# Kernel optimization log

Measured on AMD Instinct MI355X. Metric: run time of the kernel, lower is better.

The kernel has to match this reference:

```python
import jax, jax.numpy as jnp
import numpy as np

B, S, N = 16, 128, 64            # batch, sentence length, padded KB-word slots per sentence
E, DK, H, L = 128, 128, 128, 32  # char embed, kb embed, per-direction hidden (hidden_size=2H), labels
CHAR_NUM, KB_NUM = 8000, 200000


def setup_inputs():
    key = jax.random.key(0)
    ks = jax.random.split(key, 40)
    u = lambda k, sh: jax.random.uniform(k, sh, jnp.float32, -0.08, 0.08)
    inp = {
        "char_ids": jax.random.randint(ks[0], (B, S), 0, CHAR_NUM),
        "kb_word_ids": jax.random.randint(ks[1], (B, N), 0, KB_NUM),
        "word_begin": jax.random.randint(ks[2], (B, N), 0, S),
        "word_len": jax.random.randint(ks[3], (B, N), 0, 6),
        "label": jax.random.randint(ks[4], (B, S), 0, L),
        "sequence_length": jax.random.randint(ks[5], (B,), S // 2, S + 1),
        "char_emb": u(ks[6], (CHAR_NUM, E)),
        "kb_emb": u(ks[7], (KB_NUM, DK)),
        "dense_W": u(ks[8], (2 * H, L)),
        "dense_b": jnp.zeros((L,), jnp.float32),
        "crf_T": u(ks[9], (L, L)),
    }
    i = 10
    for p in ("f", "r"):
        inp[p + "_Wcx"] = u(ks[i], (E, 4 * H))
        inp[p + "_Wch"] = u(ks[i + 1], (H, 4 * H))
        inp[p + "_bc"] = jnp.zeros((4 * H,), jnp.float32)
        inp[p + "_Wwx"] = u(ks[i + 2], (DK, 3 * H))
        inp[p + "_Wwh"] = u(ks[i + 3], (H, 3 * H))
        inp[p + "_bw"] = jnp.zeros((3 * H,), jnp.float32)
        inp[p + "_Wlx"] = u(ks[i + 4], (E, H))
        inp[p + "_Wlc"] = u(ks[i + 5], (H, H))
        inp[p + "_bl"] = jnp.zeros((H,), jnp.float32)
        i += 6
    return inp


def _lattice_dir(X, Xw, begin, end, pos_valid, word_valid,
                 Wcx, Wch, bc, Wwx, Wwh, bw, Wlx, Wlc, bl):
    # X:[S,E] chars in scan order, Xw:[N,DK] KB words, begin/end:[N] span indices
    # in scan order (end inclusive), pos_valid:[S] bool, word_valid:[N] bool.
    Xg = X @ Wcx + bc    # [S,4H] hoisted char-gate input projection
    Xl = X @ Wlx + bl    # [S,H]  hoisted link-gate input projection
    Wg = Xw @ Wwx + bw   # [N,3H] hoisted word-gate input projection

    def step(carry, t):
        h_hist, c_hist = carry                 # [S+1,H]; slot k = state after step k-1
        h_prev, c_prev = h_hist[t], c_hist[t]
        gi, gf, go, gg = jnp.split(Xg[t] + h_prev @ Wch, 4)
        i = jax.nn.sigmoid(gi); f = jax.nn.sigmoid(gf)
        o = jax.nn.sigmoid(go); g = jnp.tanh(gg)
        # word cells: built from the state just before each word's begin position
        hb, cb = h_hist[begin], c_hist[begin]  # [N,H]
        wi, wf, wg = jnp.split(Wg + hb @ Wwh, 3, axis=1)
        cw = jax.nn.sigmoid(wf) * cb + jax.nn.sigmoid(wi) * jnp.tanh(wg)  # [N,H]
        lg = jax.nn.sigmoid(Xl[t] + cw @ Wlc)  # [N,H] link gates
        wmask = ((end == t) & word_valid).astype(X.dtype)[:, None]
        ew = jnp.exp(lg) * wmask
        ec = jnp.exp(i)
        c_lat = (ec * g + (ew * cw).sum(0)) / (ec + ew.sum(0))  # gate-normalized merge
        c_std = f * c_prev + i * g             # plain LSTM step when no word ends at t
        c_t = jnp.where(wmask.sum() > 0, c_lat, c_std)
        h_t = o * jnp.tanh(c_t)
        v = pos_valid[t]
        h_hist = h_hist.at[t + 1].set(jnp.where(v, h_t, h_prev))
        c_hist = c_hist.at[t + 1].set(jnp.where(v, c_t, c_prev))
        return (h_hist, c_hist), jnp.where(v, h_t, jnp.zeros_like(h_t))

    init = (jnp.zeros((S + 1, H), X.dtype), jnp.zeros((S + 1, H), X.dtype))
    _, hs = jax.lax.scan(step, init, jnp.arange(S))
    return hs  # [S,H]


def _forward(char_ids, kb_word_ids, word_begin, word_len, label, sequence_length,
             char_emb, kb_emb, dense_W, dense_b, crf_T, fparams, rparams):
    X = char_emb[char_ids]            # [B,S,E]
    Xw = kb_emb[kb_word_ids]          # [B,N,DK]
    end = jnp.minimum(word_begin + word_len, S - 1)   # inclusive span end
    word_valid = end < sequence_length[:, None]       # whole span inside sentence
    pos = jnp.arange(S)
    pv_f = pos[None, :] < sequence_length[:, None]
    fwd = jax.vmap(lambda x, xw, b, e, pv, wv:
                   _lattice_dir(x, xw, b, e, pv, wv, *fparams))(
        X, Xw, word_begin, end, pv_f, word_valid)
    # backward direction: flip time axis; span (b,e) maps to (S-1-e, S-1-b)
    pv_r = pos[None, :] >= (S - sequence_length)[:, None]
    bwd = jax.vmap(lambda x, xw, b, e, pv, wv:
                   _lattice_dir(x, xw, b, e, pv, wv, *rparams))(
        X[:, ::-1], Xw, S - 1 - end, S - 1 - word_begin, pv_r, word_valid)[:, ::-1]
    feats = jnp.concatenate([fwd, bwd], axis=-1)      # [B,S,2H]
    logits = feats @ dense_W + dense_b                # [B,S,L]
    # CRF negative log-likelihood
    mask = pv_f.astype(logits.dtype)                  # [B,S]
    emit = jnp.take_along_axis(logits, label[..., None], axis=2)[..., 0]
    trans = crf_T[label[:, :-1], label[:, 1:]]
    gold = (emit * mask).sum(1) + (trans * mask[:, 1:]).sum(1)

    def fstep(alpha, xs):
        logit_t, m_t = xs
        new = jax.scipy.special.logsumexp(alpha[:, :, None] + crf_T[None], axis=1) + logit_t
        return jnp.where(m_t[:, None] > 0, new, alpha), None

    alpha, _ = jax.lax.scan(fstep, logits[:, 0],
                            (logits[:, 1:].transpose(1, 0, 2), mask[:, 1:].T))
    logZ = jax.scipy.special.logsumexp(alpha, axis=1)
    return jnp.mean(logZ - gold)


def reference(char_ids, kb_word_ids, word_begin, word_len, label, sequence_length,
              char_emb, kb_emb, dense_W, dense_b, crf_T,
              f_Wcx, f_Wch, f_bc, f_Wwx, f_Wwh, f_bw, f_Wlx, f_Wlc, f_bl,
              r_Wcx, r_Wch, r_bc, r_Wwx, r_Wwh, r_bw, r_Wlx, r_Wlc, r_bl):
    fparams = (f_Wcx, f_Wch, f_bc, f_Wwx, f_Wwh, f_bw, f_Wlx, f_Wlc, f_bl)
    rparams = (r_Wcx, r_Wch, r_bc, r_Wwx, r_Wwh, r_bw, r_Wlx, r_Wlc, r_bl)
    return _forward(char_ids, kb_word_ids, word_begin, word_len, label, sequence_length,
                    char_emb, kb_emb, dense_W, dense_b, crf_T, fparams, rparams)
```

## Files before the change

kernel.cpp:

```cpp
#include <hip/hip_runtime.h>


typedef _Float16 f16x8 __attribute__((ext_vector_type(8)));
typedef float    f32x4 __attribute__((ext_vector_type(4)));

__device__ __forceinline__ float sigm(float x) { return 1.f / (1.f + __expf(-x)); }
__device__ __forceinline__ float tanh_fast(float x) {
    return 1.f - 2.f / (__expf(2.f * x) + 1.f);
}
__device__ __forceinline__ void bar_lgkm() {
    asm volatile("s_waitcnt lgkmcnt(0)\n\ts_barrier" ::: "memory");
}

__device__ __forceinline__ f32x4 mfma16(f16x8 a, f16x8 b, f32x4 c) {
    return __builtin_amdgcn_mfma_f32_16x16x32_f16(a, b, c, 0, 0, 0);
}

template <int K, int J, int RPB, int BLK>
__global__ __launch_bounds__(BLK)
void gemm_pair(const float* __restrict__ emb, const int* __restrict__ idx,
               const float* __restrict__ W0, const float* __restrict__ W1,
               const float* __restrict__ b0, const float* __restrict__ b1,
               float* __restrict__ out, int rowsTotal, int Sdim, int revmode)
{
    constexpr int NJ4 = J / 4;
    constexpr int RT  = BLK / NJ4;
    constexpr int RPT = RPB / RT;
    static_assert(BLK % NJ4 == 0 && RPB % RT == 0, "layout");
    const int y = blockIdx.y;
    const float* __restrict__ W    = y ? W1 : W0;
    const float* __restrict__ bias = y ? b1 : b0;
    float* __restrict__ outp = out + (size_t)y * rowsTotal * J;
    const int rev = (revmode && y) ? 1 : 0;

    __shared__ __align__(16) float xs[RPB * K];
    __shared__ const float* srcs[RPB];
    const int tid = threadIdx.x;
    const int r0 = blockIdx.x * RPB;
    if (tid < RPB) {
        const int row = r0 + tid;
        const float* s = nullptr;
        if (row < rowsTotal) {
            if (idx) {
                const int bb = row / Sdim, tt = row - bb * Sdim;
                const int ts = rev ? (Sdim - 1 - tt) : tt;
                s = emb + (size_t)idx[bb * Sdim + ts] * K;
            } else {
                s = emb + (size_t)row * K;
            }
        }
        srcs[tid] = s;
    }
    __syncthreads();
    constexpr int NQ = RPB * K / 4;
    for (int q = tid; q < NQ; q += BLK) {
        const int rr = q / (K / 4), qq = q - rr * (K / 4);
        const float4* s = (const float4*)srcs[rr];
        ((float4*)xs)[q] = s ? s[qq] : make_float4(0.f, 0.f, 0.f, 0.f);
    }
    __syncthreads();

    const int jq = tid % NJ4;
    const int rg = tid / NJ4;
    float4 acc[RPT];
#pragma unroll
    for (int r = 0; r < RPT; ++r) acc[r] = make_float4(0.f, 0.f, 0.f, 0.f);
    const float4* __restrict__ W4 = (const float4*)W;
#pragma unroll 4
    for (int k = 0; k < K; ++k) {
        const float4 wv = W4[(size_t)k * NJ4 + jq];
#pragma unroll
        for (int r = 0; r < RPT; ++r) {
            const float xv = xs[(rg * RPT + r) * K + k];
            acc[r].x = fmaf(xv, wv.x, acc[r].x);
            acc[r].y = fmaf(xv, wv.y, acc[r].y);
            acc[r].z = fmaf(xv, wv.z, acc[r].z);
            acc[r].w = fmaf(xv, wv.w, acc[r].w);
        }
    }
    const float4 bv = ((const float4*)bias)[jq];
#pragma unroll
    for (int r = 0; r < RPT; ++r) {
        const int row = r0 + rg * RPT + r;
        if (row < rowsTotal)
            ((float4*)outp)[(size_t)row * NJ4 + jq] =
                make_float4(acc[r].x + bv.x, acc[r].y + bv.y,
                            acc[r].z + bv.z, acc[r].w + bv.w);
    }
}

#define HH_BYTES (129 * 128 * 2)
#define CH_BYTES (129 * 128 * 4)
#define LAT_DYN_SMEM (HH_BYTES + CH_BYTES)

__global__ __launch_bounds__(512, 2)
void lattice_kernel(const float* __restrict__ Xg,
                    const float* __restrict__ Xl,
                    const float* __restrict__ Wgp,
                    const float* __restrict__ Wch_f, const float* __restrict__ Wch_r,
                    const float* __restrict__ Wwh_f, const float* __restrict__ Wwh_r,
                    const float* __restrict__ Wlc_f, const float* __restrict__ Wlc_r,
                    const int* __restrict__ word_begin, const int* __restrict__ word_len,
                    const int* __restrict__ seqlen,
                    float* __restrict__ feats)
{
    extern __shared__ __align__(16) char dyn_smem[];
    _Float16* hh = (_Float16*)dyn_smem;
    float*    ch = (float*)(dyn_smem + HH_BYTES);

    const int bdid = blockIdx.x;
    const int b = bdid >> 1, dir = bdid & 1;
    const int tid = threadIdx.x;
    const int wid = tid >> 6;
    const int ln  = tid & 63;
    const int lg  = ln >> 4;
    const int jm  = wid * 16 + (ln & 15);

    const float* Wch = dir ? Wch_r : Wch_f;
    const float* Wwh = dir ? Wwh_r : Wwh_f;
    const float* Wlc = dir ? Wlc_r : Wlc_f;

    f16x8 Bc[4][4];
#pragma unroll
    for (int g = 0; g < 4; ++g)
#pragma unroll
        for (int kt = 0; kt < 4; ++kt) {
            f16x8 v;
#pragma unroll
            for (int i = 0; i < 8; ++i)
                v[i] = (_Float16)Wch[(size_t)(kt * 32 + lg * 8 + i) * 512 + (g * 128 + jm)];
            Bc[g][kt] = v;
        }
    f16x8 Bw[3][4];
#pragma unroll
    for (int p = 0; p < 3; ++p)
#pragma unroll
        for (int kt = 0; kt < 4; ++kt) {
            f16x8 v;
#pragma unroll
            for (int i = 0; i < 8; ++i)
                v[i] = (_Float16)Wwh[(size_t)(kt * 32 + lg * 8 + i) * 384 + (p * 128 + jm)];
            Bw[p][kt] = v;
        }
    f16x8 Bl[4];
#pragma unroll
    for (int kt = 0; kt < 4; ++kt) {
        f16x8 v;
#pragma unroll
        for (int i = 0; i < 8; ++i)
            v[i] = (_Float16)Wlc[(size_t)(kt * 32 + lg * 8 + i) * 128 + jm];
        Bl[kt] = v;
    }

    __shared__ __align__(16) _Float16 cw2s[2][2][128];
    __shared__ int ev_start[129];
    __shared__ int cnts[128];
    __shared__ int fills[128];
    __shared__ short ev_word[64];
    __shared__ short wbeg_s[64];

    const int sl = seqlen[b];

    if (tid < 128) { cnts[tid] = 0; fills[tid] = 0; }
    __syncthreads();
    int myvalid = 0, myed = 0;
    if (tid < 64) {
        const int bg = word_begin[b * 64 + tid];
        const int lnw = word_len[b * 64 + tid];
        int ef = bg + lnw; if (ef > 127) ef = 127;
        myvalid = (ef < sl);
        const int bd_ = dir ? (127 - ef) : bg;
        const int ed_ = dir ? (127 - bg) : ef;
        wbeg_s[tid] = (short)bd_;
        myed = ed_;
        if (myvalid) atomicAdd(&cnts[ed_], 1);
    }
    __syncthreads();
    if (tid == 0) {
        int run = 0; ev_start[0] = 0;
        for (int t = 0; t < 128; ++t) { run += cnts[t]; ev_start[t + 1] = run; }
    }
    __syncthreads();
    if (tid < 64 && myvalid) {
        const int pos = atomicAdd(&fills[myed], 1);
        ev_word[ev_start[myed] + pos] = (short)tid;
    }
    if (tid < 128) { hh[tid] = (_Float16)0.f; ch[tid] = 0.f; }
    __syncthreads();

    const float* Xg_b = Xg + ((size_t)dir * 2048 + (size_t)b * 128) * 512;
    const float* Xl_b = Xl + ((size_t)dir * 2048 + (size_t)b * 128) * 128;
    const float* Wg_b = Wgp + ((size_t)dir * 1024 + (size_t)b * 64) * 384;

    float h_reg = 0.f, c_reg = 0.f;

    int   curE, cur_ec0;
    int   cur_bgs[2] = {0, 0};
    float cur_wgp[2][3] = {};
    float cur_xl = 0.f;
    float xg_cur[4];
    {
        curE = ev_start[1];
        cur_ec0 = curE < 2 ? curE : 2;
#pragma unroll
        for (int s = 0; s < 2; ++s)
            if (s < cur_ec0) {
                const int wd = ev_word[s];
                cur_bgs[s] = wbeg_s[wd];
                const float* wgr = Wg_b + (size_t)wd * 384;
                cur_wgp[s][0] = wgr[jm];
                cur_wgp[s][1] = wgr[128 + jm];
                cur_wgp[s][2] = wgr[256 + jm];
            }
        if (curE > 0) cur_xl = Xl_b[jm];
#pragma unroll
        for (int g = 0; g < 4; ++g) xg_cur[g] = Xg_b[g * 128 + jm];
    }

    for (int t = 0; t < 128; ++t) {
        int   nxtE = 0, nxt_ec0 = 0;
        int   nxt_bgs[2] = {0, 0};
        float nxt_wgp[2][3] = {};
        float nxt_xl = 0.f;
        float xg_nxt[4] = {0.f, 0.f, 0.f, 0.f};
        if (t < 127) {
            const int e0n = ev_start[t + 1];
            nxtE = ev_start[t + 2] - e0n;
            nxt_ec0 = nxtE < 2 ? nxtE : 2;
#pragma unroll
            for (int s = 0; s < 2; ++s)
                if (s < nxt_ec0) {
                    const int wd = ev_word[e0n + s];
                    nxt_bgs[s] = wbeg_s[wd];
                    const float* wgr = Wg_b + (size_t)wd * 384;
                    nxt_wgp[s][0] = wgr[jm];
                    nxt_wgp[s][1] = wgr[128 + jm];
                    nxt_wgp[s][2] = wgr[256 + jm];
                }
            if (nxtE > 0) nxt_xl = Xl_b[(size_t)(t + 1) * 128 + jm];
#pragma unroll
            for (int g = 0; g < 4; ++g)
                xg_nxt[g] = Xg_b[(size_t)(t + 1) * 512 + g * 128 + jm];
        }

        f16x8 A[4];
#pragma unroll
        for (int kt = 0; kt < 4; ++kt)
            A[kt] = ((const f16x8*)hh)[t * 16 + kt * 4 + lg];
        f32x4 d[4];
#pragma unroll
        for (int g = 0; g < 4; ++g) d[g] = (f32x4){0.f, 0.f, 0.f, 0.f};
#pragma unroll
        for (int kt = 0; kt < 4; ++kt)
#pragma unroll
            for (int g = 0; g < 4; ++g)
                d[g] = mfma16(A[kt], Bc[g][kt], d[g]);

        const float gi = sigm(d[0][0] + xg_cur[0]);
        const float gf = sigm(d[1][0] + xg_cur[1]);
        const float go = sigm(d[2][0] + xg_cur[2]);
        const float gg = tanh_fast(d[3][0] + xg_cur[3]);

        float accn = 0.f, accd = 0.f;
        if (curE > 0) {
            const int e0 = ev_start[t];
            float cwreg[2] = {0.f, 0.f};
#pragma unroll
            for (int s = 0; s < 2; ++s)
                if (s < cur_ec0) {
                    f16x8 Ab[4];
#pragma unroll
                    for (int kt = 0; kt < 4; ++kt)
                        Ab[kt] = ((const f16x8*)hh)[cur_bgs[s] * 16 + kt * 4 + lg];
                    f32x4 ep[3];
#pragma unroll
                    for (int p = 0; p < 3; ++p) ep[p] = (f32x4){0.f, 0.f, 0.f, 0.f};
#pragma unroll
                    for (int kt = 0; kt < 4; ++kt)
#pragma unroll
                        for (int p = 0; p < 3; ++p)
                            ep[p] = mfma16(Ab[kt], Bw[p][kt], ep[p]);
                    const float wi = cur_wgp[s][0] + ep[0][0];
                    const float wf = cur_wgp[s][1] + ep[1][0];
                    const float wv = cur_wgp[s][2] + ep[2][0];
                    const float cb = ch[(size_t)cur_bgs[s] * 128 + jm];
                    const float cwv = sigm(wf) * cb + sigm(wi) * tanh_fast(wv);
                    cwreg[s] = cwv;
                    if (ln < 16) cw2s[0][s][jm] = (_Float16)cwv;
                }
            bar_lgkm();
            const int nc = (curE + 1) >> 1;
            for (int c = 0; c < nc; ++c) {
                const int base2 = c * 2;
                const int en = (curE - base2) < 2 ? (curE - base2) : 2;
                float lgs[2] = {0.f, 0.f};
#pragma unroll
                for (int s = 0; s < 2; ++s)
                    if (s < en) {
                        f16x8 Ac[4];
#pragma unroll
                        for (int kt = 0; kt < 4; ++kt)
                            Ac[kt] = ((const f16x8*)(&cw2s[c & 1][s][0]))[kt * 4 + lg];
                        f32x4 r = (f32x4){0.f, 0.f, 0.f, 0.f};
#pragma unroll
                        for (int kt = 0; kt < 4; ++kt)
                            r = mfma16(Ac[kt], Bl[kt], r);
                        lgs[s] = r[0];
                    }
                const int nb = base2 + 2;
                int nn = curE - nb; nn = nn < 0 ? 0 : (nn > 2 ? 2 : nn);
                float cwn[2] = {0.f, 0.f};
#pragma unroll
                for (int s = 0; s < 2; ++s)
                    if (s < nn) {
                        const int wd = ev_word[e0 + nb + s];
                        const int bg2 = wbeg_s[wd];
                        const float* wgr = Wg_b + (size_t)wd * 384;
                        const float wg0 = wgr[jm], wg1 = wgr[128 + jm], wg2 = wgr[256 + jm];
                        f16x8 Ab[4];
#pragma unroll
                        for (int kt = 0; kt < 4; ++kt)
                            Ab[kt] = ((const f16x8*)hh)[bg2 * 16 + kt * 4 + lg];
                        f32x4 ep[3];
#pragma unroll
                        for (int p = 0; p < 3; ++p) ep[p] = (f32x4){0.f, 0.f, 0.f, 0.f};
#pragma unroll
                        for (int kt = 0; kt < 4; ++kt)
#pragma unroll
                            for (int p = 0; p < 3; ++p)
                                ep[p] = mfma16(Ab[kt], Bw[p][kt], ep[p]);
                        const float wi = wg0 + ep[0][0];
                        const float wf = wg1 + ep[1][0];
                        const float wv = wg2 + ep[2][0];
                        const float cb = ch[(size_t)bg2 * 128 + jm];
                        const float cwv = sigm(wf) * cb + sigm(wi) * tanh_fast(wv);
                        cwn[s] = cwv;
                        if (ln < 16) cw2s[(c + 1) & 1][s][jm] = (_Float16)cwv;
                    }
#pragma unroll
                for (int s = 0; s < 2; ++s)
                    if (s < en) {
                        const float lgv = sigm(cur_xl + lgs[s]);
                        const float ew = __expf(lgv);
                        accn = fmaf(ew, cwreg[s], accn);
                        accd += ew;
                    }
                if (c + 1 < nc) {
                    bar_lgkm();
                    cwreg[0] = cwn[0]; cwreg[1] = cwn[1];
                }
            }
        }

        float c_t;
        if (curE > 0) {
            const float ec = __expf(gi);
            c_t = (ec * gg + accn) / (ec + accd);
        } else {
            c_t = gf * c_reg + gi * gg;
        }
        const float h_t = go * tanh_fast(c_t);
        const bool v = dir ? (t >= 128 - sl) : (t < sl);
        const float hn = v ? h_t : h_reg;
        const float cn = v ? c_t : c_reg;
        h_reg = hn; c_reg = cn;
        if (ln < 16) {
            hh[(size_t)(t + 1) * 128 + jm] = (_Float16)hn;
            ch[(size_t)(t + 1) * 128 + jm] = cn;
        }

        curE = nxtE; cur_ec0 = nxt_ec0;
        cur_bgs[0] = nxt_bgs[0]; cur_bgs[1] = nxt_bgs[1];
#pragma unroll
        for (int s = 0; s < 2; ++s) {
            cur_wgp[s][0] = nxt_wgp[s][0];
            cur_wgp[s][1] = nxt_wgp[s][1];
            cur_wgp[s][2] = nxt_wgp[s][2];
        }
        cur_xl = nxt_xl;
#pragma unroll
        for (int g = 0; g < 4; ++g) xg_cur[g] = xg_nxt[g];
        bar_lgkm();
    }

    for (int i = tid; i < 128 * 128; i += 512) {
        const int t = i >> 7, j = i & 127;
        const bool v = dir ? (t >= 128 - sl) : (t < sl);
        const float hv = v ? (float)hh[(size_t)(t + 1) * 128 + j] : 0.f;
        const int s = dir ? (127 - t) : t;
        feats[((size_t)b * 128 + s) * 256 + dir * 128 + j] = hv;
    }
}

__global__ void crf_kernel(const float* __restrict__ logits,
                           const int* __restrict__ label,
                           const int* __restrict__ seqlen,
                           const float* __restrict__ T,
                           float* __restrict__ out_part)
{
    const int half = threadIdx.x >> 5;
    const int j    = threadIdx.x & 31;
    const int b    = blockIdx.x * 2 + half;

    float Tc[32];
#pragma unroll
    for (int i = 0; i < 32; ++i) Tc[i] = T[i * 32 + j];

    const float* lg = logits + (size_t)b * 128 * 32;
    const int* lab = label + b * 128;
    const int sl = seqlen[b];

    float g = 0.f;
#pragma unroll
    for (int r = 0; r < 4; ++r) {
        const int t = j + r * 32;
        if (t < sl) {
            g += lg[t * 32 + lab[t]];
            if (t >= 1) g += T[lab[t - 1] * 32 + lab[t]];
        }
    }
#pragma unroll
    for (int m = 16; m; m >>= 1) g += __shfl_xor(g, m, 32);

    __shared__ __align__(16) float alpha_s[2][32];
    float av = lg[j];
    alpha_s[half][j] = av;
    __syncthreads();
    for (int t = 1; t < 128; ++t) {
        float a[32];
        const float4* ap = (const float4*)alpha_s[half];
#pragma unroll
        for (int q = 0; q < 8; ++q) {
            const float4 v = ap[q];
            a[4 * q] = v.x; a[4 * q + 1] = v.y; a[4 * q + 2] = v.z; a[4 * q + 3] = v.w;
        }
        float m = -1e30f;
#pragma unroll
        for (int i = 0; i < 32; ++i) m = fmaxf(m, a[i] + Tc[i]);
        float s = 0.f;
#pragma unroll
        for (int i = 0; i < 32; ++i) s += __expf(a[i] + Tc[i] - m);
        float nv = m + __logf(s) + lg[t * 32 + j];
        if (t >= sl) nv = av;
        av = nv;
        __syncthreads();
        alpha_s[half][j] = av;
        __syncthreads();
    }
    float m2 = av;
#pragma unroll
    for (int m = 16; m; m >>= 1) m2 = fmaxf(m2, __shfl_xor(m2, m, 32));
    float s2 = __expf(av - m2);
#pragma unroll
    for (int m = 16; m; m >>= 1) s2 += __shfl_xor(s2, m, 32);
    if (j == 0) out_part[b] = (m2 + __logf(s2)) - g;
}

__global__ void finalize_kernel(const float* __restrict__ partb, float* __restrict__ out)
{
    if (threadIdx.x == 0 && blockIdx.x == 0) {
        float s = 0.f;
        for (int i = 0; i < 16; i++) s += partb[i];
        out[0] = s * (1.f / 16.f);
    }
}

extern "C" void kernel_launch(void* const* d_in, const int* in_sizes, int n_in,
                              void* d_out, int out_size, void* d_ws, size_t ws_size,
                              hipStream_t stream)
{
    (void)in_sizes; (void)n_in; (void)out_size; (void)ws_size;
    const int*   char_ids    = (const int*)d_in[0];
    const int*   kb_word_ids = (const int*)d_in[1];
    const int*   word_begin  = (const int*)d_in[2];
    const int*   word_len    = (const int*)d_in[3];
    const int*   label       = (const int*)d_in[4];
    const int*   seqlen      = (const int*)d_in[5];
    const float* char_emb    = (const float*)d_in[6];
    const float* kb_emb      = (const float*)d_in[7];
    const float* dense_W     = (const float*)d_in[8];
    const float* dense_b     = (const float*)d_in[9];
    const float* crf_T       = (const float*)d_in[10];
    const float* f_Wcx = (const float*)d_in[11];
    const float* f_Wch = (const float*)d_in[12];
    const float* f_bc  = (const float*)d_in[13];
    const float* f_Wwx = (const float*)d_in[14];
    const float* f_Wwh = (const float*)d_in[15];
    const float* f_bw  = (const float*)d_in[16];
    const float* f_Wlx = (const float*)d_in[17];
    const float* f_Wlc = (const float*)d_in[18];
    const float* f_bl  = (const float*)d_in[19];
    const float* r_Wcx = (const float*)d_in[20];
    const float* r_Wch = (const float*)d_in[21];
    const float* r_bc  = (const float*)d_in[22];
    const float* r_Wwx = (const float*)d_in[23];
    const float* r_Wwh = (const float*)d_in[24];
    const float* r_bw  = (const float*)d_in[25];
    const float* r_Wlx = (const float*)d_in[26];
    const float* r_Wlc = (const float*)d_in[27];
    const float* r_bl  = (const float*)d_in[28];

    float* ws = (float*)d_ws;
    size_t o = 0;
    float* Xg     = ws + o; o += (size_t)2 * 2048 * 512;
    float* Xl     = ws + o; o += (size_t)2 * 2048 * 128;
    float* Wg     = ws + o; o += (size_t)2 * 1024 * 384;
    float* feats  = ws + o; o += (size_t)2048 * 256;
    float* logits = ws + o; o += (size_t)2048 * 32;
    float* partb  = ws + o; o += 16;

    gemm_pair<128, 512, 8, 256><<<dim3(256, 2), 256, 0, stream>>>(
        char_emb, char_ids, f_Wcx, r_Wcx, f_bc, r_bc, Xg, 2048, 128, 1);
    gemm_pair<128, 128, 8, 256><<<dim3(256, 2), 256, 0, stream>>>(
        char_emb, char_ids, f_Wlx, r_Wlx, f_bl, r_bl, Xl, 2048, 128, 1);
    gemm_pair<128, 384, 8, 192><<<dim3(128, 2), 192, 0, stream>>>(
        kb_emb, kb_word_ids, f_Wwx, r_Wwx, f_bw, r_bw, Wg, 1024, 64, 0);

    lattice_kernel<<<32, 512, LAT_DYN_SMEM, stream>>>(
        Xg, Xl, Wg, f_Wch, r_Wch, f_Wwh, r_Wwh, f_Wlc, r_Wlc,
        word_begin, word_len, seqlen, feats);

    gemm_pair<256, 32, 16, 128><<<dim3(128, 1), 128, 0, stream>>>(
        feats, nullptr, dense_W, dense_W, dense_b, dense_b, logits, 2048, 128, 0);
    crf_kernel<<<8, 64, 0, stream>>>(logits, label, seqlen, crf_T, partb);
    finalize_kernel<<<1, 64, 0, stream>>>(partb, (float*)d_out);
}
```

Before: 518.6 us.

## Halve lattice block to 4 waves, each wave computing two 16-column tiles

The lattice recurrence kernel now runs 256 threads (4 waves) per block instead of 512, and each wave handles two 16-column output tiles. Weight fragments, gate inputs and states are duplicated per tile. Fewer waves should make each per-step barrier cheaper and let every wave reuse its A-operand loads across two MFMAs. The cost is twice the register-held weights per thread, which risks spills, and more serial MFMA and elementwise work per wave on the critical path.

```diff
diff --git a/kernel.cpp b/kernel.cpp
--- a/kernel.cpp
+++ b/kernel.cpp
@@ -93,7 +93,7 @@
 #define CH_BYTES (129 * 128 * 4)
 #define LAT_DYN_SMEM (HH_BYTES + CH_BYTES)
 
-__global__ __launch_bounds__(512, 2)
+__global__ __launch_bounds__(256, 1)
 void lattice_kernel(const float* __restrict__ Xg,
                     const float* __restrict__ Xl,
                     const float* __restrict__ Wgp,
@@ -114,43 +114,54 @@
     const int wid = tid >> 6;
     const int ln  = tid & 63;
     const int lg  = ln >> 4;
-    const int jm  = wid * 16 + (ln & 15);
+    const int c15 = ln & 15;
+    const int jm0 = wid * 32 + c15;
+    const int jm1 = jm0 + 16;
 
     const float* Wch = dir ? Wch_r : Wch_f;
     const float* Wwh = dir ? Wwh_r : Wwh_f;
     const float* Wlc = dir ? Wlc_r : Wlc_f;
 
-    f16x8 Bc[4][4];
+    f16x8 Bc[4][2][4];
 #pragma unroll
     for (int g = 0; g < 4; ++g)
 #pragma unroll
+        for (int ct = 0; ct < 2; ++ct)
+#pragma unroll
+            for (int kt = 0; kt < 4; ++kt) {
+                const int col = g * 128 + (ct ? jm1 : jm0);
+                f16x8 v;
+#pragma unroll
+                for (int i = 0; i < 8; ++i)
+                    v[i] = (_Float16)Wch[(size_t)(kt * 32 + lg * 8 + i) * 512 + col];
+                Bc[g][ct][kt] = v;
+            }
+    f16x8 Bw[3][2][4];
+#pragma unroll
+    for (int p = 0; p < 3; ++p)
+#pragma unroll
+        for (int ct = 0; ct < 2; ++ct)
+#pragma unroll
+            for (int kt = 0; kt < 4; ++kt) {
+                const int col = p * 128 + (ct ? jm1 : jm0);
+                f16x8 v;
+#pragma unroll
+                for (int i = 0; i < 8; ++i)
+                    v[i] = (_Float16)Wwh[(size_t)(kt * 32 + lg * 8 + i) * 384 + col];
+                Bw[p][ct][kt] = v;
+            }
+    f16x8 Bl[2][4];
+#pragma unroll
+    for (int ct = 0; ct < 2; ++ct)
+#pragma unroll
         for (int kt = 0; kt < 4; ++kt) {
+            const int col = ct ? jm1 : jm0;
             f16x8 v;
 #pragma unroll
             for (int i = 0; i < 8; ++i)
-                v[i] = (_Float16)Wch[(size_t)(kt * 32 + lg * 8 + i) * 512 + (g * 128 + jm)];
-            Bc[g][kt] = v;
-        }
-    f16x8 Bw[3][4];
-#pragma unroll
-    for (int p = 0; p < 3; ++p)
-#pragma unroll
-        for (int kt = 0; kt < 4; ++kt) {
-            f16x8 v;
-#pragma unroll
-            for (int i = 0; i < 8; ++i)
-                v[i] = (_Float16)Wwh[(size_t)(kt * 32 + lg * 8 + i) * 384 + (p * 128 + jm)];
-            Bw[p][kt] = v;
-        }
-    f16x8 Bl[4];
-#pragma unroll
-    for (int kt = 0; kt < 4; ++kt) {
-        f16x8 v;
-#pragma unroll
-        for (int i = 0; i < 8; ++i)
-            v[i] = (_Float16)Wlc[(size_t)(kt * 32 + lg * 8 + i) * 128 + jm];
-        Bl[kt] = v;
-    }
+                v[i] = (_Float16)Wlc[(size_t)(kt * 32 + lg * 8 + i) * 128 + col];
+            Bl[ct][kt] = v;
+        }
 
     __shared__ __align__(16) _Float16 cw2s[2][2][128];
     __shared__ int ev_start[129];
@@ -192,13 +203,13 @@
     const float* Xl_b = Xl + ((size_t)dir * 2048 + (size_t)b * 128) * 128;
     const float* Wg_b = Wgp + ((size_t)dir * 1024 + (size_t)b * 64) * 384;
 
-    float h_reg = 0.f, c_reg = 0.f;
+    float h_reg[2] = {0.f, 0.f}, c_reg[2] = {0.f, 0.f};
 
     int   curE, cur_ec0;
     int   cur_bgs[2] = {0, 0};
-    float cur_wgp[2][3] = {};
-    float cur_xl = 0.f;
-    float xg_cur[4];
+    float cur_wgp[2][3][2] = {};
+    float cur_xl[2] = {0.f, 0.f};
+    float xg_cur[4][2];
     {
         curE = ev_start[1];
         cur_ec0 = curE < 2 ? curE : 2;
@@ -208,21 +219,26 @@
                 const int wd = ev_word[s];
                 cur_bgs[s] = wbeg_s[wd];
                 const float* wgr = Wg_b + (size_t)wd * 384;
-                cur_wgp[s][0] = wgr[jm];
-                cur_wgp[s][1] = wgr[128 + jm];
-                cur_wgp[s][2] = wgr[256 + jm];
-            }
-        if (curE > 0) cur_xl = Xl_b[jm];
-#pragma unroll
-        for (int g = 0; g < 4; ++g) xg_cur[g] = Xg_b[g * 128 + jm];
+#pragma unroll
+                for (int p = 0; p < 3; ++p) {
+                    cur_wgp[s][p][0] = wgr[p * 128 + jm0];
+                    cur_wgp[s][p][1] = wgr[p * 128 + jm1];
+                }
+            }
+        if (curE > 0) { cur_xl[0] = Xl_b[jm0]; cur_xl[1] = Xl_b[jm1]; }
+#pragma unroll
+        for (int g = 0; g < 4; ++g) {
+            xg_cur[g][0] = Xg_b[g * 128 + jm0];
+            xg_cur[g][1] = Xg_b[g * 128 + jm1];
+        }
     }
 
     for (int t = 0; t < 128; ++t) {
         int   nxtE = 0, nxt_ec0 = 0;
         int   nxt_bgs[2] = {0, 0};
-        float nxt_wgp[2][3] = {};
-        float nxt_xl = 0.f;
-        float xg_nxt[4] = {0.f, 0.f, 0.f, 0.f};
+        float nxt_wgp[2][3][2] = {};
+        float nxt_xl[2] = {0.f, 0.f};
+        float xg_nxt[4][2] = {};
         if (t < 127) {
             const int e0n = ev_start[t + 1];
             nxtE = ev_start[t + 2] - e0n;
@@ -233,38 +249,53 @@
                     const int wd = ev_word[e0n + s];
                     nxt_bgs[s] = wbeg_s[wd];
                     const float* wgr = Wg_b + (size_t)wd * 384;
-                    nxt_wgp[s][0] = wgr[jm];
-                    nxt_wgp[s][1] = wgr[128 + jm];
-                    nxt_wgp[s][2] = wgr[256 + jm];
+#pragma unroll
+                    for (int p = 0; p < 3; ++p) {
+                        nxt_wgp[s][p][0] = wgr[p * 128 + jm0];
+                        nxt_wgp[s][p][1] = wgr[p * 128 + jm1];
+                    }
                 }
-            if (nxtE > 0) nxt_xl = Xl_b[(size_t)(t + 1) * 128 + jm];
-#pragma unroll
-            for (int g = 0; g < 4; ++g)
-                xg_nxt[g] = Xg_b[(size_t)(t + 1) * 512 + g * 128 + jm];
+            if (nxtE > 0) {
+                nxt_xl[0] = Xl_b[(size_t)(t + 1) * 128 + jm0];
+                nxt_xl[1] = Xl_b[(size_t)(t + 1) * 128 + jm1];
+            }
+#pragma unroll
+            for (int g = 0; g < 4; ++g) {
+                xg_nxt[g][0] = Xg_b[(size_t)(t + 1) * 512 + g * 128 + jm0];
+                xg_nxt[g][1] = Xg_b[(size_t)(t + 1) * 512 + g * 128 + jm1];
+            }
         }
 
         f16x8 A[4];
 #pragma unroll
         for (int kt = 0; kt < 4; ++kt)
             A[kt] = ((const f16x8*)hh)[t * 16 + kt * 4 + lg];
-        f32x4 d[4];
-#pragma unroll
-        for (int g = 0; g < 4; ++g) d[g] = (f32x4){0.f, 0.f, 0.f, 0.f};
+        f32x4 d[4][2];
+#pragma unroll
+        for (int g = 0; g < 4; ++g)
+#pragma unroll
+            for (int ct = 0; ct < 2; ++ct) d[g][ct] = (f32x4){0.f, 0.f, 0.f, 0.f};
 #pragma unroll
         for (int kt = 0; kt < 4; ++kt)
 #pragma unroll
             for (int g = 0; g < 4; ++g)
-                d[g] = mfma16(A[kt], Bc[g][kt], d[g]);
-
-        const float gi = sigm(d[0][0] + xg_cur[0]);
-        const float gf = sigm(d[1][0] + xg_cur[1]);
-        const float go = sigm(d[2][0] + xg_cur[2]);
-        const float gg = tanh_fast(d[3][0] + xg_cur[3]);
-
-        float accn = 0.f, accd = 0.f;
+#pragma unroll
+                for (int ct = 0; ct < 2; ++ct)
+                    d[g][ct] = mfma16(A[kt], Bc[g][ct][kt], d[g][ct]);
+
+        float gi[2], gf[2], go[2], gg[2];
+#pragma unroll
+        for (int ct = 0; ct < 2; ++ct) {
+            gi[ct] = sigm(d[0][ct][0] + xg_cur[0][ct]);
+            gf[ct] = sigm(d[1][ct][0] + xg_cur[1][ct]);
+            go[ct] = sigm(d[2][ct][0] + xg_cur[2][ct]);
+            gg[ct] = tanh_fast(d[3][ct][0] + xg_cur[3][ct]);
+        }
+
+        float accn[2] = {0.f, 0.f}, accd[2] = {0.f, 0.f};
         if (curE > 0) {
             const int e0 = ev_start[t];
-            float cwreg[2] = {0.f, 0.f};
+            float cwreg[2][2] = {};
 #pragma unroll
             for (int s = 0; s < 2; ++s)
                 if (s < cur_ec0) {
@@ -272,28 +303,36 @@
 #pragma unroll
                     for (int kt = 0; kt < 4; ++kt)
                         Ab[kt] = ((const f16x8*)hh)[cur_bgs[s] * 16 + kt * 4 + lg];
-                    f32x4 ep[3];
-#pragma unroll
-                    for (int p = 0; p < 3; ++p) ep[p] = (f32x4){0.f, 0.f, 0.f, 0.f};
+                    f32x4 ep[3][2];
+#pragma unroll
+                    for (int p = 0; p < 3; ++p)
+#pragma unroll
+                        for (int ct = 0; ct < 2; ++ct) ep[p][ct] = (f32x4){0.f, 0.f, 0.f, 0.f};
 #pragma unroll
                     for (int kt = 0; kt < 4; ++kt)
 #pragma unroll
                         for (int p = 0; p < 3; ++p)
-                            ep[p] = mfma16(Ab[kt], Bw[p][kt], ep[p]);
-                    const float wi = cur_wgp[s][0] + ep[0][0];
-                    const float wf = cur_wgp[s][1] + ep[1][0];
-                    const float wv = cur_wgp[s][2] + ep[2][0];
-                    const float cb = ch[(size_t)cur_bgs[s] * 128 + jm];
-                    const float cwv = sigm(wf) * cb + sigm(wi) * tanh_fast(wv);
-                    cwreg[s] = cwv;
-                    if (ln < 16) cw2s[0][s][jm] = (_Float16)cwv;
+#pragma unroll
+                            for (int ct = 0; ct < 2; ++ct)
+                                ep[p][ct] = mfma16(Ab[kt], Bw[p][ct][kt], ep[p][ct]);
+#pragma unroll
+                    for (int ct = 0; ct < 2; ++ct) {
+                        const int col = ct ? jm1 : jm0;
+                        const float wi = cur_wgp[s][0][ct] + ep[0][ct][0];
+                        const float wf = cur_wgp[s][1][ct] + ep[1][ct][0];
+                        const float wv = cur_wgp[s][2][ct] + ep[2][ct][0];
+                        const float cb = ch[(size_t)cur_bgs[s] * 128 + col];
+                        const float cwv = sigm(wf) * cb + sigm(wi) * tanh_fast(wv);
+                        cwreg[s][ct] = cwv;
+                        if (lg == 0) cw2s[0][s][col] = (_Float16)cwv;
+                    }
                 }
             bar_lgkm();
             const int nc = (curE + 1) >> 1;
             for (int c = 0; c < nc; ++c) {
                 const int base2 = c * 2;
                 const int en = (curE - base2) < 2 ? (curE - base2) : 2;
-                float lgs[2] = {0.f, 0.f};
+                float lgs[2][2] = {};
 #pragma unroll
                 for (int s = 0; s < 2; ++s)
                     if (s < en) {
@@ -301,89 +340,113 @@
 #pragma unroll
                         for (int kt = 0; kt < 4; ++kt)
                             Ac[kt] = ((const f16x8*)(&cw2s[c & 1][s][0]))[kt * 4 + lg];
-                        f32x4 r = (f32x4){0.f, 0.f, 0.f, 0.f};
-#pragma unroll
-                        for (int kt = 0; kt < 4; ++kt)
-                            r = mfma16(Ac[kt], Bl[kt], r);
-                        lgs[s] = r[0];
+                        f32x4 r[2];
+                        r[0] = (f32x4){0.f, 0.f, 0.f, 0.f};
+                        r[1] = (f32x4){0.f, 0.f, 0.f, 0.f};
+#pragma unroll
+                        for (int kt = 0; kt < 4; ++kt) {
+                            r[0] = mfma16(Ac[kt], Bl[0][kt], r[0]);
+                            r[1] = mfma16(Ac[kt], Bl[1][kt], r[1]);
+                        }
+                        lgs[s][0] = r[0][0]; lgs[s][1] = r[1][0];
                     }
                 const int nb = base2 + 2;
                 int nn = curE - nb; nn = nn < 0 ? 0 : (nn > 2 ? 2 : nn);
-                float cwn[2] = {0.f, 0.f};
+                float cwn[2][2] = {};
 #pragma unroll
                 for (int s = 0; s < 2; ++s)
                     if (s < nn) {
                         const int wd = ev_word[e0 + nb + s];
                         const int bg2 = wbeg_s[wd];
                         const float* wgr = Wg_b + (size_t)wd * 384;
-                        const float wg0 = wgr[jm], wg1 = wgr[128 + jm], wg2 = wgr[256 + jm];
                         f16x8 Ab[4];
 #pragma unroll
                         for (int kt = 0; kt < 4; ++kt)
                             Ab[kt] = ((const f16x8*)hh)[bg2 * 16 + kt * 4 + lg];
-                        f32x4 ep[3];
-#pragma unroll
-                        for (int p = 0; p < 3; ++p) ep[p] = (f32x4){0.f, 0.f, 0.f, 0.f};
+                        f32x4 ep[3][2];
+#pragma unroll
+                        for (int p = 0; p < 3; ++p)
+#pragma unroll
+                            for (int ct = 0; ct < 2; ++ct) ep[p][ct] = (f32x4){0.f, 0.f, 0.f, 0.f};
 #pragma unroll
                         for (int kt = 0; kt < 4; ++kt)
 #pragma unroll
                             for (int p = 0; p < 3; ++p)
-                                ep[p] = mfma16(Ab[kt], Bw[p][kt], ep[p]);
-                        const float wi = wg0 + ep[0][0];
-                        const float wf = wg1 + ep[1][0];
-                        const float wv = wg2 + ep[2][0];
-                        const float cb = ch[(size_t)bg2 * 128 + jm];
-                        const float cwv = sigm(wf) * cb + sigm(wi) * tanh_fast(wv);
-                        cwn[s] = cwv;
-                        if (ln < 16) cw2s[(c + 1) & 1][s][jm] = (_Float16)cwv;
+#pragma unroll
+                                for (int ct = 0; ct < 2; ++ct)
+                                    ep[p][ct] = mfma16(Ab[kt], Bw[p][ct][kt], ep[p][ct]);
+#pragma unroll
+                        for (int ct = 0; ct < 2; ++ct) {
+                            const int col = ct ? jm1 : jm0;
+                            const float wi = wgr[col] + ep[0][ct][0];
+                            const float wf = wgr[128 + col] + ep[1][ct][0];
+                            const float wv = wgr[256 + col] + ep[2][ct][0];
+                            const float cb = ch[(size_t)bg2 * 128 + col];
+                            const float cwv = sigm(wf) * cb + sigm(wi) * tanh_fast(wv);
+                            cwn[s][ct] = cwv;
+                            if (lg == 0) cw2s[(c + 1) & 1][s][col] = (_Float16)cwv;
+                        }
                     }
 #pragma unroll
                 for (int s = 0; s < 2; ++s)
-                    if (s < en) {
-                        const float lgv = sigm(cur_xl + lgs[s]);
-                        const float ew = __expf(lgv);
-                        accn = fmaf(ew, cwreg[s], accn);
-                        accd += ew;
-                    }
+                    if (s < en)
+#pragma unroll
+                        for (int ct = 0; ct < 2; ++ct) {
+                            const float lgv = sigm(cur_xl[ct] + lgs[s][ct]);
+                            const float ew = __expf(lgv);
+                            accn[ct] = fmaf(ew, cwreg[s][ct], accn[ct]);
+                            accd[ct] += ew;
+                        }
                 if (c + 1 < nc) {
                     bar_lgkm();
-                    cwreg[0] = cwn[0]; cwreg[1] = cwn[1];
+#pragma unroll
+                    for (int s = 0; s < 2; ++s)
+#pragma unroll
+                        for (int ct = 0; ct < 2; ++ct) cwreg[s][ct] = cwn[s][ct];
                 }
             }
         }
 
-        float c_t;
-        if (curE > 0) {
-            const float ec = __expf(gi);
-            c_t = (ec * gg + accn) / (ec + accd);
-        } else {
-            c_t = gf * c_reg + gi * gg;
-        }
-        const float h_t = go * tanh_fast(c_t);
-        const bool v = dir ? (t >= 128 - sl) : (t < sl);
-        const float hn = v ? h_t : h_reg;
-        const float cn = v ? c_t : c_reg;
-        h_reg = hn; c_reg = cn;
-        if (ln < 16) {
-            hh[(size_t)(t + 1) * 128 + jm] = (_Float16)hn;
-            ch[(size_t)(t + 1) * 128 + jm] = cn;
+#pragma unroll
+        for (int ct = 0; ct < 2; ++ct) {
+            float c_t;
+            if (curE > 0) {
+                const float ec = __expf(gi[ct]);
+                c_t = (ec * gg[ct] + accn[ct]) / (ec + accd[ct]);
+            } else {
+                c_t = gf[ct] * c_reg[ct] + gi[ct] * gg[ct];
+            }
+            const float h_t = go[ct] * tanh_fast(c_t);
+            const bool v = dir ? (t >= 128 - sl) : (t < sl);
+            const float hn = v ? h_t : h_reg[ct];
+            const float cn = v ? c_t : c_reg[ct];
+            h_reg[ct] = hn; c_reg[ct] = cn;
+            if (lg == 0) {
+                const int col = ct ? jm1 : jm0;
+                hh[(size_t)(t + 1) * 128 + col] = (_Float16)hn;
+                ch[(size_t)(t + 1) * 128 + col] = cn;
+            }
         }
 
         curE = nxtE; cur_ec0 = nxt_ec0;
         cur_bgs[0] = nxt_bgs[0]; cur_bgs[1] = nxt_bgs[1];
 #pragma unroll
-        for (int s = 0; s < 2; ++s) {
-            cur_wgp[s][0] = nxt_wgp[s][0];
-            cur_wgp[s][1] = nxt_wgp[s][1];
-            cur_wgp[s][2] = nxt_wgp[s][2];
-        }
-        cur_xl = nxt_xl;
-#pragma unroll
-        for (int g = 0; g < 4; ++g) xg_cur[g] = xg_nxt[g];
+        for (int s = 0; s < 2; ++s)
+#pragma unroll
+            for (int p = 0; p < 3; ++p) {
+                cur_wgp[s][p][0] = nxt_wgp[s][p][0];
+                cur_wgp[s][p][1] = nxt_wgp[s][p][1];
+            }
+        cur_xl[0] = nxt_xl[0]; cur_xl[1] = nxt_xl[1];
+#pragma unroll
+        for (int g = 0; g < 4; ++g) {
+            xg_cur[g][0] = xg_nxt[g][0];
+            xg_cur[g][1] = xg_nxt[g][1];
+        }
         bar_lgkm();
     }
 
-    for (int i = tid; i < 128 * 128; i += 512) {
+    for (int i = tid; i < 128 * 128; i += 256) {
         const int t = i >> 7, j = i & 127;
         const bool v = dir ? (t >= 128 - sl) : (t < sl);
         const float hv = v ? (float)hh[(size_t)(t + 1) * 128 + j] : 0.f;
@@ -516,7 +579,7 @@
     gemm_pair<128, 384, 8, 192><<<dim3(128, 2), 192, 0, stream>>>(
         kb_emb, kb_word_ids, f_Wwx, r_Wwx, f_bw, r_bw, Wg, 1024, 64, 0);
 
-    lattice_kernel<<<32, 512, LAT_DYN_SMEM, stream>>>(
+    lattice_kernel<<<32, 256, LAT_DYN_SMEM, stream>>>(
         Xg, Xl, Wg, f_Wch, r_Wch, f_Wwh, r_Wwh, f_Wlc, r_Wlc,
         word_begin, word_len, seqlen, feats);
 
```

Result: slower. 603.0 us (+16.3%).
